# Optimization experiments

Measured on AMD Instinct MI355X. Metric: run time of the kernel, lower is better.

Reference implementation:

```python
import jax, jax.numpy as jnp
import numpy as np
from jax.scipy.special import logsumexp

B, L, M, D = 8192, 1024, 128, 2  # batch, hilbert.size, bond dim, local_size
MACHINE_POW = 2


def setup_inputs() -> dict:
    key = jax.random.key(0)
    k1, k2 = jax.random.split(key)
    # configurations in the zero-magnetization sector: each row is a permutation
    # of L//2 zeros and L//2 ones (constrained HomogeneousHilbert)
    base = jnp.tile(jnp.arange(D, dtype=jnp.int32), L // D)  # (L,)
    inputs = jax.vmap(lambda k: jax.random.permutation(k, base))(jax.random.split(k1, B))
    # variational parameters epsilon: (local_size, M, size); centered at 1 so the
    # length-L multiplicative cache chain stays in fp32 range
    epsilon = 1.0 + 0.02 * jax.random.normal(k2, (D, M, L), dtype=jnp.float32)
    return {"inputs": inputs, "epsilon": epsilon}


def _conditionals(inputs, epsilon):
    # inputs: (B, L) int in [0, D); epsilon: (D, M, L)
    Bn, Ln = inputs.shape
    Dn, Mn, _ = epsilon.shape
    half = Ln // 2

    def scan_fun(carry, index):
        cache, n_spins = carry                       # (B, D, M), (B, D)
        prev = inputs[:, (index - 1) % Ln]           # (B,) previous-site state
        params_i = epsilon[:, :, index]              # (D, M)
        # irregular gather: cache[b, prev[b], :]
        gathered = jnp.take_along_axis(cache, prev[:, None, None], axis=1)[:, 0, :]  # (B, M)
        prods = params_i[None, :, :] * gathered[:, None, :]  # (B, D, M)
        log_psi = jnp.sum(prods, axis=-1)            # (B, D) sum over bond dim
        n_spins = jnp.where(index > 0,
                            n_spins + jax.nn.one_hot(prev, Dn, dtype=jnp.int32),
                            n_spins)
        # zero-magnetization renormalization: -inf once a local state is exhausted
        renorm = jnp.log(jnp.heaviside((half - n_spins).astype(log_psi.dtype), 0.0))
        return (prods, n_spins), log_psi + renorm

    cache0 = jnp.ones((Bn, Dn, Mn), epsilon.dtype)
    n0 = jnp.zeros((Bn, Dn), jnp.int32)
    _, log_psi = jax.lax.scan(scan_fun, (cache0, n0), jnp.arange(Ln))
    return jnp.transpose(log_psi, (1, 0, 2))  # (B, L, D)


def reference(inputs, epsilon):
    lp = _conditionals(inputs, epsilon)  # (B, L, D)
    # normalize conditionals over local states (machine_pow = 2)
    lp = lp - (1.0 / MACHINE_POW) * logsumexp(MACHINE_POW * lp, axis=-1, keepdims=True)
    # pick the log-conditional of the actual configuration at each site
    sel = jnp.take_along_axis(lp, inputs[:, :, None], axis=2)[:, :, 0]  # (B, L)
    # n_symm = 1 (default apply_symmetries): symmetrized logsumexp is identity
    return jnp.sum(sel, axis=1)  # (B,) log_psi
```

## Files before the change

### kernel.cpp

```cpp
#include <hip/hip_runtime.h>
#include <hip/hip_fp16.h>

typedef unsigned long long u64;
typedef unsigned int uint32;
typedef short short8 __attribute__((ext_vector_type(8)));
typedef float f32x4 __attribute__((ext_vector_type(4)));
typedef _Float16 h2 __attribute__((ext_vector_type(2)));

#define B_N 8192
#define L_N 1024
#define M_N 128
#define C_N 16
#define CH_N 64
#define HALF_N 512

#define OFF_W16  0
#define OFF_R16  0x40000
#define OFF_BITS 0x80000
#define OFF_LR   0x180000
#define OFF_RQ   0x1C0000
#define OFF_T    0x21C0000

#define PACK_BLK 2048
#define PACK_IT  16
#define EPS_BLK  32
#define ZERO_BLK 32

__device__ __forceinline__ unsigned short f32_bf16(float f) {
    union { float f; unsigned u; } x; x.f = f;
    unsigned u = x.u + 0x7FFFu + ((x.u >> 16) & 1u);
    return (unsigned short)(u >> 16);
}

__device__ __forceinline__ float fdot2(h2 a, h2 b, float c) {
#if __has_builtin(__builtin_amdgcn_fdot2)
    return __builtin_amdgcn_fdot2(a, b, c, false);
#else
    return (float)a[0] * (float)b[0] + (float)a[1] * (float)b[1] + c;
#endif
}

__device__ __forceinline__ uint32 fas_u(float f) { union { float f; uint32 u; } x; x.f = f; return x.u; }
__device__ __forceinline__ float uas_f(uint32 u) { union { uint32 u; float f; } x; x.u = u; return x.f; }

template<int CTRL>
__device__ __forceinline__ float dpp_add(float x, float y) {
    union { float f; int i; } a, r;
    a.f = y;
    r.i = __builtin_amdgcn_update_dpp(0, a.i, CTRL, 0xF, 0xF, true);
    return x + r.f;
}

union HU { uint32 u; __half2 hh; h2 v2; };

__global__ __launch_bounds__(256) void k_prep(const int* __restrict__ inp,
        const float* __restrict__ eps, u64* __restrict__ bits,
        _Float16* __restrict__ w16, _Float16* __restrict__ r16,
        unsigned short* __restrict__ lrT, float* __restrict__ out) {
    int bid = blockIdx.x;
    if (bid < PACK_BLK) {
        int g = bid * 256 + threadIdx.x;
        const int stride = PACK_BLK * 256;
        #pragma unroll 4
        for (int it = 0; it < PACK_IT; ++it) {
            int v = inp[g];
            u64 m = __ballot(v != 0);
            if ((threadIdx.x & 63) == 0) bits[g >> 6] = m;
            g += stride;
        }
        return;
    }
    bid -= PACK_BLK;
    if (bid < EPS_BLK) {
        int wid = threadIdx.x >> 6, lane = threadIdx.x & 63;
        int m = bid * 4 + wid;
        const float* e0 = eps + (size_t)m * L_N + lane * 16;
        const float* e1 = eps + (size_t)(M_N + m) * L_N + lane * 16;
        float a[16], b[16];
        #pragma unroll
        for (int j = 0; j < 16; j += 4) {
            *(float4*)&a[j] = *(const float4*)&e0[j];
            *(float4*)&b[j] = *(const float4*)&e1[j];
        }
        float local = 1.f;
        #pragma unroll
        for (int j = 0; j < 16; ++j) local *= a[j];
        float sc = local;
        #pragma unroll
        for (int d = 1; d < 64; d <<= 1) {
            float up = __shfl_up(sc, d);
            if (lane >= d) sc *= up;
        }
        float prev = __shfl_up(sc, 1);
        float E = (lane == 0) ? 1.f : prev;
        int i0 = lane * 16;
        #pragma unroll
        for (int j = 0; j < 16; ++j) {
            float rat = b[j] / a[j];
            w16[(size_t)(i0 + j) * M_N + m] = (_Float16)(E * (a[j] - b[j]));
            r16[(size_t)(i0 + j) * M_N + m] = (_Float16)(rat - 1.f);
            lrT[(size_t)m * L_N + i0 + j] = f32_bf16(__log2f(rat));
            E *= a[j];
        }
        return;
    }
    bid -= EPS_BLK;
    if (bid < ZERO_BLK) {
        out[bid * 256 + threadIdx.x] = 0.f;
    }
}

__global__ __launch_bounds__(256) void k_slog2(const u64* __restrict__ bits,
        const unsigned short* __restrict__ lrT, _Float16* __restrict__ Rq,
        int* __restrict__ T) {
    if (blockIdx.x >= 1024) {
        int b = (blockIdx.x - 1024) * 256 + threadIdx.x;
        const u64* brow = bits + (size_t)b * 16;
        int n1 = 0, n0 = 0, Tv = 1024;
        for (int wd = 0; wd < 16; ++wd) {
            u64 x = brow[wd];
            int pc = __popcll(x);
            if (n1 + pc < HALF_N && n0 + (64 - pc) < HALF_N) {
                n1 += pc; n0 += 64 - pc;
                continue;
            }
            int found = 0;
            for (int k = 0; k < 64; ++k) {
                if (n1 >= HALF_N || n0 >= HALF_N) { Tv = wd * 64 + k; found = 1; break; }
                int sb = (int)((x >> k) & 1);
                n1 += sb; n0 += 1 - sb;
            }
            if (!found) Tv = (wd + 1) * 64;
            break;
        }
        T[b] = Tv;
        return;
    }
    int btile = blockIdx.x >> 1;
    int half = blockIdx.x & 1;
    int wid = threadIdx.x >> 6, lane = threadIdx.x & 63;
    int col = lane & 15, quad = lane >> 4;
    int m = (half * 4 + wid) * 16 + col;
    int b_row = btile * 16 + col;
    const u64* brow = bits + (size_t)b_row * 16;
    const unsigned short* lrow = lrT + (size_t)m * L_N;

    f32x4 cum = (f32x4){0.f, 0.f, 0.f, 0.f};

    for (int c = 0; c < C_N; ++c) {
        #pragma unroll
        for (int reg = 0; reg < 4; ++reg) {
            int b = btile * 16 + quad * 4 + reg;
            Rq[((size_t)c * B_N + b) * M_N + m] = (_Float16)exp2f(cum[reg]);
        }
        u64 wv = brow[c];
        short8 a0, a1;
        #pragma unroll
        for (int j = 0; j < 8; ++j) {
            a0[j] = (short)((((wv >> (quad * 8 + j)) & 1) != 0) ? 0x3F80 : 0);
            a1[j] = (short)((((wv >> (32 + quad * 8 + j)) & 1) != 0) ? 0x3F80 : 0);
        }
        const unsigned short* bp = lrow + c * 64 + quad * 8;
        union { uint4 u; short8 s; } bf0, bf1;
        bf0.u = *(const uint4*)bp;
        bf1.u = *(const uint4*)(bp + 32);
        cum = __builtin_amdgcn_mfma_f32_16x16x32_bf16(a0, bf0.s, cum, 0, 0, 0);
        cum = __builtin_amdgcn_mfma_f32_16x16x32_bf16(a1, bf1.s, cum, 0, 0, 0);
    }
}

__global__ __launch_bounds__(256, 2) void k_main(const u64* __restrict__ bits,
        const _Float16* __restrict__ w16, const _Float16* __restrict__ r16,
        const _Float16* __restrict__ Rq, const int* __restrict__ T,
        float* __restrict__ out) {
    __shared__ _Float16 wbuf[CH_N * M_N];
    __shared__ _Float16 rbuf[CH_N * M_N];
    int c = blockIdx.x & (C_N - 1);
    int bblk = blockIdx.x >> 4;
    int lane = threadIdx.x & 63, wid = threadIdx.x >> 6;
    int s = lane & 7, g = lane >> 3;
    int b0 = bblk * 64 + wid * 16 + g * 2;
    int b_own = b0 + (s & 1);

    {
        const uint4* sw = (const uint4*)(w16 + (size_t)c * CH_N * M_N);
        const uint4* sr = (const uint4*)(r16 + (size_t)c * CH_N * M_N);
        uint4* dw = (uint4*)wbuf; uint4* dr = (uint4*)rbuf;
        #pragma unroll
        for (int t = 0; t < 4; ++t) {
            dw[threadIdx.x + t * 256] = sw[threadIdx.x + t * 256];
            dr[threadIdx.x + t * 256] = sr[threadIdx.x + t * 256];
        }
    }

    HU R2[2][8];
    #pragma unroll
    for (int nb = 0; nb < 2; ++nb) {
        union { uint4 q[2]; uint32 w[8]; } P;
        const uint4* src = (const uint4*)(Rq + ((size_t)c * B_N + (b0 + nb)) * M_N + s * 16);
        P.q[0] = src[0]; P.q[1] = src[1];
        #pragma unroll
        for (int j = 0; j < 8; ++j) R2[nb][j].u = P.w[j];
    }
    int Tb = T[b_own];
    u64 wb[2];
    wb[0] = bits[(size_t)b0 * 16 + c];
    wb[1] = bits[(size_t)(b0 + 1) * 16 + c];

    __syncthreads();

    const float LOG2E2 = 2.885390082f;
    const float NHL2 = -0.3465735903f;
    float sum = 0.f;
    #pragma unroll
    for (int h = 0; h < 2; ++h) {
        uint32 wh[2];
        wh[0] = (uint32)(wb[0] >> (h * 32));
        wh[1] = (uint32)(wb[1] >> (h * 32));
        uint32 ows = ~((s & 1) ? wh[1] : wh[0]);
        int rel = Tb - (c * CH_N + h * 32);
        uint32 vmask = (rel <= 0) ? 0u : ((rel >= 32) ? 0xFFFFFFFFu : ((1u << rel) - 1u));

        for (int tt = 0; tt < 32; ++tt) {
            int base = (h * 32 + tt) * M_N + s * 16;
            union { uint4 q[2]; uint32 w[8]; h2 v2[8]; } W, Rm;
            W.q[0] = *(const uint4*)&wbuf[base];
            W.q[1] = *((const uint4*)&wbuf[base] + 1);
            Rm.q[0] = *(const uint4*)&rbuf[base];
            Rm.q[1] = *((const uint4*)&rbuf[base] + 1);

            float d[2];
            #pragma unroll
            for (int nb = 0; nb < 2; ++nb) {
                float acc = 0.f;
                #pragma unroll
                for (int j = 0; j < 8; ++j) acc = fdot2(R2[nb][j].v2, W.v2[j], acc);
                d[nb] = acc;
            }
            float xa = (s & 1) ? d[1] : d[0];
            float ya = (s & 1) ? d[0] : d[1];
            xa = dpp_add<0xB1>(xa, ya);
            xa = dpp_add<0x4E>(xa, xa);
            xa = dpp_add<0x104>(xa, xa);

            uint32 sgn = (ows << (31 - tt)) & 0x80000000u;
            float y = uas_f(fas_u(xa) ^ sgn);
            float contr = NHL2 * __log2f(1.f + exp2f(LOG2E2 * y));
            int vm = (int)(vmask << (31 - tt)) >> 31;
            sum += uas_f(fas_u(contr) & (uint32)vm);

            #pragma unroll
            for (int nb = 0; nb < 2; ++nb) {
                uint32 msk = (uint32)((int)(wh[nb] << (31 - tt)) >> 31);
                #pragma unroll
                for (int j = 0; j < 8; ++j) {
                    HU sel; sel.u = Rm.w[j] & msk;
                    R2[nb][j].v2 += sel.v2 * R2[nb][j].v2;
                }
            }
        }
    }
    if (s < 2) atomicAdd(&out[b_own], sum);
}

extern "C" void kernel_launch(void* const* d_in, const int* in_sizes, int n_in,
                              void* d_out, int out_size, void* d_ws, size_t ws_size,
                              hipStream_t stream) {
    const int*   inputs  = (const int*)d_in[0];
    const float* epsilon = (const float*)d_in[1];
    float* out = (float*)d_out;

    char* ws = (char*)d_ws;
    _Float16* w16 = (_Float16*)(ws + OFF_W16);
    _Float16* r16 = (_Float16*)(ws + OFF_R16);
    u64*   bits   = (u64*)  (ws + OFF_BITS);
    unsigned short* lrT = (unsigned short*)(ws + OFF_LR);
    _Float16* Rq  = (_Float16*)(ws + OFF_RQ);
    int*   T      = (int*)  (ws + OFF_T);

    k_prep<<<PACK_BLK + EPS_BLK + ZERO_BLK, 256, 0, stream>>>(
        inputs, epsilon, bits, w16, r16, lrT, out);
    k_slog2<<<1024 + 32, 256, 0, stream>>>(bits, lrT, Rq, T);
    k_main<<<(B_N / 64) * C_N, 256, 0, stream>>>(bits, w16, r16, Rq, T, out);
}
```

Baseline: 179.8 us.

## Remap k_main lanes to 16 per batch group of 4 and raise occupancy

Each batch group now spans 16 lanes, each holding 8 bond elements for 4 batch rows instead of 16 elements for 2 rows. Per-thread register state stays the same size, but the shared-memory loads per step halve and the cross-lane reduction becomes a 4-way butterfly over 16 lanes. Launch bounds are raised from 2 to 4 blocks per CU to increase occupancy. This adds more DPP reduction steps and may cause register spilling under the tighter register limit.

```diff
diff --git a/kernel.cpp b/kernel.cpp
--- a/kernel.cpp
+++ b/kernel.cpp
@@ -169,7 +169,7 @@
     }
 }
 
-__global__ __launch_bounds__(256, 2) void k_main(const u64* __restrict__ bits,
+__global__ __launch_bounds__(256, 4) void k_main(const u64* __restrict__ bits,
         const _Float16* __restrict__ w16, const _Float16* __restrict__ r16,
         const _Float16* __restrict__ Rq, const int* __restrict__ T,
         float* __restrict__ out) {
@@ -178,9 +178,9 @@
     int c = blockIdx.x & (C_N - 1);
     int bblk = blockIdx.x >> 4;
     int lane = threadIdx.x & 63, wid = threadIdx.x >> 6;
-    int s = lane & 7, g = lane >> 3;
-    int b0 = bblk * 64 + wid * 16 + g * 2;
-    int b_own = b0 + (s & 1);
+    int s = lane & 15, row = lane >> 4;
+    int q = s & 3;
+    int b0 = bblk * 64 + wid * 16 + row * 4;
 
     {
         const uint4* sw = (const uint4*)(w16 + (size_t)c * CH_N * M_N);
@@ -193,19 +193,18 @@
         }
     }
 
-    HU R2[2][8];
+    HU R2[4][4];
+    u64 wb[4];
     #pragma unroll
-    for (int nb = 0; nb < 2; ++nb) {
-        union { uint4 q[2]; uint32 w[8]; } P;
-        const uint4* src = (const uint4*)(Rq + ((size_t)c * B_N + (b0 + nb)) * M_N + s * 16);
-        P.q[0] = src[0]; P.q[1] = src[1];
-        #pragma unroll
-        for (int j = 0; j < 8; ++j) R2[nb][j].u = P.w[j];
-    }
-    int Tb = T[b_own];
-    u64 wb[2];
-    wb[0] = bits[(size_t)b0 * 16 + c];
-    wb[1] = bits[(size_t)(b0 + 1) * 16 + c];
+    for (int k = 0; k < 4; ++k) {
+        int b = b0 + (q ^ k);
+        union { uint4 v; uint32 w[4]; } P;
+        P.v = *(const uint4*)(Rq + ((size_t)c * B_N + b) * M_N + s * 8);
+        #pragma unroll
+        for (int j = 0; j < 4; ++j) R2[k][j].u = P.w[j];
+        wb[k] = bits[(size_t)b * 16 + c];
+    }
+    int Tb = T[b0 + q];
 
     __syncthreads();
 
@@ -214,53 +213,51 @@
     float sum = 0.f;
     #pragma unroll
     for (int h = 0; h < 2; ++h) {
-        uint32 wh[2];
-        wh[0] = (uint32)(wb[0] >> (h * 32));
-        wh[1] = (uint32)(wb[1] >> (h * 32));
-        uint32 ows = ~((s & 1) ? wh[1] : wh[0]);
+        uint32 wh[4];
+        #pragma unroll
+        for (int k = 0; k < 4; ++k) wh[k] = (uint32)(wb[k] >> (h * 32));
+        uint32 ows = ~wh[0];
         int rel = Tb - (c * CH_N + h * 32);
         uint32 vmask = (rel <= 0) ? 0u : ((rel >= 32) ? 0xFFFFFFFFu : ((1u << rel) - 1u));
 
         for (int tt = 0; tt < 32; ++tt) {
-            int base = (h * 32 + tt) * M_N + s * 16;
-            union { uint4 q[2]; uint32 w[8]; h2 v2[8]; } W, Rm;
-            W.q[0] = *(const uint4*)&wbuf[base];
-            W.q[1] = *((const uint4*)&wbuf[base] + 1);
-            Rm.q[0] = *(const uint4*)&rbuf[base];
-            Rm.q[1] = *((const uint4*)&rbuf[base] + 1);
-
-            float d[2];
+            int base = (h * 32 + tt) * M_N + s * 8;
+            union { uint4 q4; uint32 w[4]; h2 v2[4]; } W, Rm;
+            W.q4 = *(const uint4*)&wbuf[base];
+            Rm.q4 = *(const uint4*)&rbuf[base];
+
+            float d[4];
             #pragma unroll
-            for (int nb = 0; nb < 2; ++nb) {
+            for (int k = 0; k < 4; ++k) {
                 float acc = 0.f;
                 #pragma unroll
-                for (int j = 0; j < 8; ++j) acc = fdot2(R2[nb][j].v2, W.v2[j], acc);
-                d[nb] = acc;
-            }
-            float xa = (s & 1) ? d[1] : d[0];
-            float ya = (s & 1) ? d[0] : d[1];
-            xa = dpp_add<0xB1>(xa, ya);
-            xa = dpp_add<0x4E>(xa, xa);
-            xa = dpp_add<0x104>(xa, xa);
+                for (int j = 0; j < 4; ++j) acc = fdot2(R2[k][j].v2, W.v2[j], acc);
+                d[k] = acc;
+            }
+            float xa = dpp_add<0xB1>(d[0], d[1]);
+            float xb = dpp_add<0xB1>(d[2], d[3]);
+            float uD = dpp_add<0x4E>(xa, xb);
+            uD = dpp_add<0x108>(uD, uD);
+            uD = dpp_add<0x104>(uD, uD);
 
             uint32 sgn = (ows << (31 - tt)) & 0x80000000u;
-            float y = uas_f(fas_u(xa) ^ sgn);
+            float y = uas_f(fas_u(uD) ^ sgn);
             float contr = NHL2 * __log2f(1.f + exp2f(LOG2E2 * y));
             int vm = (int)(vmask << (31 - tt)) >> 31;
             sum += uas_f(fas_u(contr) & (uint32)vm);
 
             #pragma unroll
-            for (int nb = 0; nb < 2; ++nb) {
-                uint32 msk = (uint32)((int)(wh[nb] << (31 - tt)) >> 31);
+            for (int k = 0; k < 4; ++k) {
+                uint32 msk = (uint32)((int)(wh[k] << (31 - tt)) >> 31);
                 #pragma unroll
-                for (int j = 0; j < 8; ++j) {
+                for (int j = 0; j < 4; ++j) {
                     HU sel; sel.u = Rm.w[j] & msk;
-                    R2[nb][j].v2 += sel.v2 * R2[nb][j].v2;
+                    R2[k][j].v2 += sel.v2 * R2[k][j].v2;
                 }
             }
         }
     }
-    if (s < 2) atomicAdd(&out[b_own], sum);
+    if (s < 4) atomicAdd(&out[b0 + s], sum);
 }
 
 extern "C" void kernel_launch(void* const* d_in, const int* in_sizes, int n_in,
```

New measurement: 184.6 us. 1.03x slower.
